# Optimization experiments

Hardware: AMD Instinct MI355X
Metric: run time of the kernel (lower is better)

Reference implementation:

```python
import jax, jax.numpy as jnp
import numpy as np
from jax import lax

B, C, H, W = 32, 128, 56, 56
O, KS, K = 128, 3, 2
HIDDEN = 32  # int(in_planes * ratio)
TEMPERATURE = 31.0
STRIDE, PAD = 1, 1


def setup_inputs() -> dict:
    key = jax.random.key(0)
    ks = jax.random.split(key, 6)
    return {
        "x": jax.random.normal(ks[0], (B, C, H, W), jnp.float32),
        "common_weight": jax.random.normal(ks[1], (1, O, C, KS, KS), jnp.float32) * 0.05,
        "common_bias": jax.random.normal(ks[2], (1, O), jnp.float32) * 0.05,
        "dyn_weight": jax.random.normal(ks[3], (1, O, C, KS, KS), jnp.float32) * 0.05,
        "dyn_bias": jnp.zeros((1, O), jnp.float32),
        "fc1_w": jax.random.normal(ks[4], (HIDDEN, C), jnp.float32) * 0.1,
        "fc2_w": jax.random.normal(ks[5], (K, HIDDEN), jnp.float32) * 0.1,
    }


def reference(x, common_weight, common_bias, dyn_weight, dyn_bias, fc1_w, fc2_w):
    b, c, h, w = x.shape
    # attention2d: global avg pool -> 1x1 conv -> relu -> 1x1 conv -> softmax(./T)
    pooled = jnp.mean(x, axis=(2, 3))                       # [B, C]
    hid = jax.nn.relu(pooled @ fc1_w.T)                     # [B, hidden]
    logits = hid @ fc2_w.T                                  # [B, K]
    attn = jax.nn.softmax(logits / TEMPERATURE, axis=1)     # [B, K]

    # aggregate per-sample weights/biases from the K-bank
    weight_all = jnp.concatenate([common_weight, dyn_weight], axis=0)  # [K,O,C,k,k]
    agg_w = jnp.einsum('bk,kocij->bocij', attn, weight_all)            # [B,O,C,k,k]
    bias_all = jnp.concatenate([common_bias, dyn_bias], axis=0)       # [K,O]
    agg_b = attn @ bias_all                                            # [B,O]

    # per-sample conv via grouped conv with feature_group_count = batch
    x1 = x.reshape(1, b * c, h, w)
    w1 = agg_w.reshape(b * O, c, KS, KS)
    out = lax.conv_general_dilated(
        x1, w1,
        window_strides=(STRIDE, STRIDE),
        padding=((PAD, PAD), (PAD, PAD)),
        dimension_numbers=('NCHW', 'OIHW', 'NCHW'),
        feature_group_count=b,
    )  # [1, B*O, H', W']
    out = out.reshape(b, O, out.shape[-2], out.shape[-1])
    return out + agg_b[:, :, None, None]
```

## Files before the change

### kernel.cpp

```cpp
#include <hip/hip_runtime.h>


#define B_ 32
#define C_ 128
#define O_ 128
#define SP_ 3136

typedef __bf16  bf16x8 __attribute__((ext_vector_type(8)));
typedef short   short8 __attribute__((ext_vector_type(8)));
typedef float   f32x4  __attribute__((ext_vector_type(4)));

__device__ __forceinline__ short f2bf(float f) {
  unsigned u = __float_as_uint(f);
  u += 0x7fffu + ((u >> 16) & 1u);
  return (short)(u >> 16);
}
__device__ __forceinline__ float bf2f(short s) {
  return __uint_as_float(((unsigned)(unsigned short)s) << 16);
}

#define GLOAD_LDS16(gp, lp)                                                     \
  __builtin_amdgcn_global_load_lds(                                             \
      (const __attribute__((address_space(1))) unsigned int*)(gp),              \
      (__attribute__((address_space(3))) unsigned int*)(lp), 16, 0, 0)

#define WS_PARTIAL_F 0
#define WS_ATTN_F    229376
#define WS_AGGB_F    229440
#define WS_ZERO_B    934144
#define WS_WB_B      935168
#define WS_XH_B      10372352
#define WS_NEED      36062464ull

__global__ __launch_bounds__(256) void convert_k(const float* __restrict__ x,
                                                 short* __restrict__ xh,
                                                 float* __restrict__ partial) {
  const int h = blockIdx.x, b = blockIdx.y;
  const int tid = threadIdx.x;
  __shared__ short lc[C_ * 57];
  const float* xp = x + (size_t)b * C_ * SP_ + h * 56;
#pragma unroll
  for (int q = 0; q < 7; ++q) {
    int i = q * 256 + tid;
    int c = i / 14, w4 = (i - c * 14) * 4;
    float4 v = *reinterpret_cast<const float4*>(xp + (size_t)c * SP_ + w4);
    lc[c * 57 + w4 + 0] = f2bf(v.x);
    lc[c * 57 + w4 + 1] = f2bf(v.y);
    lc[c * 57 + w4 + 2] = f2bf(v.z);
    lc[c * 57 + w4 + 3] = f2bf(v.w);
  }
  __syncthreads();
  if (tid < C_) {
    float s = 0.f;
    for (int w = 0; w < 56; ++w) s += bf2f(lc[tid * 57 + w]);
    partial[((size_t)b * 56 + h) * C_ + tid] = s;
  }
  short* xo = xh + ((size_t)b * 56 + h) * 56 * C_;
  for (int u = tid; u < 896; u += 256) {
    int w = u >> 4, cp = (u & 15) * 8;
    short8 v;
#pragma unroll
    for (int k = 0; k < 8; ++k) v[k] = lc[(cp + k) * 57 + w];
    *reinterpret_cast<short8*>(xo + w * C_ + cp) = v;
  }
}

__global__ __launch_bounds__(256) void pool_attn_k(const float* __restrict__ partial,
                                                   const float* __restrict__ fc1,
                                                   const float* __restrict__ fc2,
                                                   const float* __restrict__ cbias,
                                                   const float* __restrict__ dbias,
                                                   float* __restrict__ attn,
                                                   float* __restrict__ aggb) {
  const int b = blockIdx.x, tid = threadIdx.x;
  __shared__ float red[256];
  __shared__ float pooled_s[C_];
  __shared__ float hid[32];
  __shared__ float at[2];
  {
    const int c = tid & 127, half = tid >> 7;
    float s = 0.f;
    for (int hh = half * 28; hh < half * 28 + 28; ++hh)
      s += partial[((size_t)b * 56 + hh) * C_ + c];
    red[tid] = s;
  }
  __syncthreads();
  if (tid < C_) pooled_s[tid] = (red[tid] + red[tid + 128]) * (1.f / 3136.f);
  __syncthreads();
  if (tid < 32) {
    float s = 0.f;
    for (int c = 0; c < C_; ++c) s += pooled_s[c] * fc1[tid * C_ + c];
    hid[tid] = fmaxf(s, 0.f);
  }
  __syncthreads();
  if (tid == 0) {
    float l0 = 0.f, l1 = 0.f;
    for (int hh = 0; hh < 32; ++hh) {
      l0 += hid[hh] * fc2[hh];
      l1 += hid[hh] * fc2[32 + hh];
    }
    l0 *= (1.f / 31.f); l1 *= (1.f / 31.f);
    float m = fmaxf(l0, l1);
    float e0 = __expf(l0 - m), e1 = __expf(l1 - m);
    float inv = 1.f / (e0 + e1);
    at[0] = e0 * inv; at[1] = e1 * inv;
    attn[b * 2] = at[0]; attn[b * 2 + 1] = at[1];
  }
  __syncthreads();
  if (tid < C_)
    aggb[b * O_ + tid] = at[0] * cbias[tid] + at[1] * dbias[tid];
}

__global__ __launch_bounds__(256) void wagg_k(const float* __restrict__ w0,
                                              const float* __restrict__ w1,
                                              const float* __restrict__ attn,
                                              short* __restrict__ Wb) {
  const int b = blockIdx.x >> 3, og = blockIdx.x & 7;
  const int o0 = og * 16;
  const int tid = threadIdx.x;
  const float a0 = attn[b * 2], a1 = attn[b * 2 + 1];
  __shared__ short wl[9 * 16 * C_];
#pragma unroll
  for (int it = 0; it < 8; ++it) {
    int r = it * 256 + tid;
    int o = o0 + (r >> 7), c = r & 127;
    size_t base = ((size_t)o * C_ + c) * 9;
#pragma unroll
    for (int j = 0; j < 9; ++j) {
      float v = a0 * w0[base + j] + a1 * w1[base + j];
      wl[j * 2048 + r] = f2bf(v);
    }
  }
  __syncthreads();
#pragma unroll
  for (int it = 0; it < 9; ++it) {
    int u = it * 256 + tid;
    int ij = u >> 8, v = (u & 255) * 8;
    *reinterpret_cast<short8*>(Wb + (((size_t)b * 9 + ij) * O_ + o0) * C_ + v) =
        *reinterpret_cast<const short8*>(&wl[ij * 2048 + v]);
  }
}

#define TPOS 348
#define UNITS 1392
#define BUFB 22272
__global__ __launch_bounds__(256) void conv2_k(const char* __restrict__ wsbase,
                                               const short* __restrict__ Wb,
                                               const float* __restrict__ aggb,
                                               float* __restrict__ out) {
  const int flat = blockIdx.x;
  const int swz = (flat & 7) * 56 + (flat >> 3);
  const int b = swz / 14, ht = swz - b * 14;
  const int h0 = ht * 4;
  const int tid = threadIdx.x;
  const int lane = tid & 63, wv = tid >> 6;
  const int obase = (wv >> 1) * 64;
  const int nbase = (wv & 1) * 112;
  const int l15 = lane & 15, g = lane >> 4;

  __shared__ short xs[2 * BUFB / 2];

  int goff[6];
  bool gact[6];
#pragma unroll
  for (int it = 0; it < 6; ++it) {
    int u = tid + it * 256;
    gact[it] = (u < UNITS);
    int uu = gact[it] ? u : 0;
    int pos = uu >> 2;
    int spart = ((uu & 3) - (uu >> 4)) & 3;
    int r = pos / 58, wc = pos - r * 58;
    int h = h0 - 1 + r, w = wc - 1;
    bool val = (unsigned)h < 56u && (unsigned)w < 56u;
    goff[it] = val ? (int)(WS_XH_B + 2 * (((((b * 56 + h) * 56 + w)) << 7) + spart * 8))
                   : (int)WS_ZERO_B;
  }

  int ptile[7];
#pragma unroll
  for (int n = 0; n < 7; ++n) {
    int p = nbase + n * 16 + l15;
    int hl = p / 56, wl = p - hl * 56;
    ptile[n] = (hl + 1) * 58 + (wl + 1);
  }

  f32x4 acc[4][7];
#pragma unroll
  for (int m = 0; m < 4; ++m)
#pragma unroll
    for (int n = 0; n < 7; ++n) acc[m][n] = f32x4{0.f, 0.f, 0.f, 0.f};

#pragma unroll
  for (int it = 0; it < 6; ++it)
    if (gact[it])
      GLOAD_LDS16(wsbase + goff[it], (char*)xs + it * 4096 + wv * 1024);
  __syncthreads();

#pragma unroll
  for (int cc = 0; cc < 4; ++cc) {
    const int cur = cc & 1;
    if (cc < 3) {
      const int nb = cur ^ 1;
#pragma unroll
      for (int it = 0; it < 6; ++it)
        if (gact[it])
          GLOAD_LDS16(wsbase + goff[it] + (cc + 1) * 64,
                      (char*)xs + nb * BUFB + it * 4096 + wv * 1024);
    }
    const char* bp = (const char*)xs + cur * BUFB;
    const short* wbb = Wb + (((size_t)b * 9) << 14) + cc * 32 + g * 8;
#pragma unroll
    for (int ij = 0; ij < 9; ++ij) {
      const int sh = (ij / 3 - 1) * 58 + (ij % 3 - 1);
      bf16x8 af[4];
#pragma unroll
      for (int m = 0; m < 4; ++m)
        af[m] = *reinterpret_cast<const bf16x8*>(wbb + (ij << 14) + (obase + m * 16 + l15) * C_);
#pragma unroll
      for (int n = 0; n < 7; ++n) {
        int pp = ptile[n] + sh;
        int off = (pp << 6) + ((((pp >> 2) + g) & 3) << 4);
        bf16x8 bfr = *reinterpret_cast<const bf16x8*>(bp + off);
#pragma unroll
        for (int m = 0; m < 4; ++m)
          acc[m][n] = __builtin_amdgcn_mfma_f32_16x16x32_bf16(af[m], bfr, acc[m][n], 0, 0, 0);
      }
    }
    __syncthreads();
  }

  const int r4 = g * 4;
#pragma unroll
  for (int m = 0; m < 4; ++m) {
    float bias[4];
#pragma unroll
    for (int j = 0; j < 4; ++j) bias[j] = aggb[b * O_ + obase + m * 16 + r4 + j];
#pragma unroll
    for (int n = 0; n < 7; ++n) {
      int p = nbase + n * 16 + l15;
      int h = h0 + p / 56, w = p % 56;
#pragma unroll
      for (int j = 0; j < 4; ++j) {
        int o = obase + m * 16 + r4 + j;
        out[((size_t)(b * O_ + o) * 56 + h) * 56 + w] = acc[m][n][j] + bias[j];
      }
    }
  }
}

extern "C" void kernel_launch(void* const* d_in, const int* in_sizes, int n_in,
                              void* d_out, int out_size, void* d_ws, size_t ws_size,
                              hipStream_t stream) {
  const float* x    = (const float*)d_in[0];
  const float* cw   = (const float*)d_in[1];
  const float* cb   = (const float*)d_in[2];
  const float* dw   = (const float*)d_in[3];
  const float* db   = (const float*)d_in[4];
  const float* fc1  = (const float*)d_in[5];
  const float* fc2  = (const float*)d_in[6];
  float* out = (float*)d_out;

  char* wsb     = (char*)d_ws;
  float* partial = (float*)wsb + WS_PARTIAL_F;
  float* attn    = (float*)wsb + WS_ATTN_F;
  float* aggb    = (float*)wsb + WS_AGGB_F;
  short* Wb      = (short*)(wsb + WS_WB_B);
  short* xh      = (short*)(wsb + WS_XH_B);

  hipMemsetAsync(wsb + WS_ZERO_B, 0, 1024, stream);
  convert_k<<<dim3(56, B_), 256, 0, stream>>>(x, xh, partial);
  pool_attn_k<<<B_, 256, 0, stream>>>(partial, fc1, fc2, cb, db, attn, aggb);
  wagg_k<<<256, 256, 0, stream>>>(cw, dw, attn, Wb);
  conv2_k<<<448, 256, 0, stream>>>(wsb, Wb, aggb, out);
}
```

Baseline: 179.4 us.

## Stage conv weight tiles through double-buffered LDS and parallelize attention MLP

New measurement: 175.4 us. 1.02x faster.

```diff
diff --git a/kernel.cpp b/kernel.cpp
--- a/kernel.cpp
+++ b/kernel.cpp
@@ -30,7 +30,6 @@
 #define WS_ZERO_B    934144
 #define WS_WB_B      935168
 #define WS_XH_B      10372352
-#define WS_NEED      36062464ull
 
 __global__ __launch_bounds__(256) void convert_k(const float* __restrict__ x,
                                                  short* __restrict__ xh,
@@ -76,6 +75,7 @@
   __shared__ float red[256];
   __shared__ float pooled_s[C_];
   __shared__ float hid[32];
+  __shared__ float lg[2];
   __shared__ float at[2];
   {
     const int c = tid & 127, half = tid >> 7;
@@ -87,21 +87,38 @@
   __syncthreads();
   if (tid < C_) pooled_s[tid] = (red[tid] + red[tid + 128]) * (1.f / 3136.f);
   __syncthreads();
+  {
+    const int hd = tid >> 3, part = tid & 7;
+    const float4* fa = reinterpret_cast<const float4*>(fc1 + hd * C_ + part * 16);
+    const float4* pa = reinterpret_cast<const float4*>(pooled_s + part * 16);
+    float s = 0.f;
+#pragma unroll
+    for (int i = 0; i < 4; ++i) {
+      float4 f = fa[i], p = pa[i];
+      s += f.x * p.x + f.y * p.y + f.z * p.z + f.w * p.w;
+    }
+    red[tid] = s;
+  }
+  __syncthreads();
   if (tid < 32) {
-    float s = 0.f;
-    for (int c = 0; c < C_; ++c) s += pooled_s[c] * fc1[tid * C_ + c];
-    hid[tid] = fmaxf(s, 0.f);
+    float v = 0.f;
+#pragma unroll
+    for (int j = 0; j < 8; ++j) v += red[tid * 8 + j];
+    hid[tid] = fmaxf(v, 0.f);
+  }
+  __syncthreads();
+  if (tid < 64) red[tid] = hid[tid & 31] * fc2[tid];
+  __syncthreads();
+  if (tid < 2) {
+    float l = 0.f;
+#pragma unroll
+    for (int hh = 0; hh < 32; ++hh) l += red[tid * 32 + hh];
+    lg[tid] = l * (1.f / 31.f);
   }
   __syncthreads();
   if (tid == 0) {
-    float l0 = 0.f, l1 = 0.f;
-    for (int hh = 0; hh < 32; ++hh) {
-      l0 += hid[hh] * fc2[hh];
-      l1 += hid[hh] * fc2[32 + hh];
-    }
-    l0 *= (1.f / 31.f); l1 *= (1.f / 31.f);
-    float m = fmaxf(l0, l1);
-    float e0 = __expf(l0 - m), e1 = __expf(l1 - m);
+    float m = fmaxf(lg[0], lg[1]);
+    float e0 = __expf(lg[0] - m), e1 = __expf(lg[1] - m);
     float inv = 1.f / (e0 + e1);
     at[0] = e0 * inv; at[1] = e1 * inv;
     attn[b * 2] = at[0]; attn[b * 2 + 1] = at[1];
@@ -142,12 +159,13 @@
 }
 
 #define TPOS 348
-#define UNITS 1392
-#define BUFB 22272
-__global__ __launch_bounds__(256) void conv2_k(const char* __restrict__ wsbase,
-                                               const short* __restrict__ Wb,
-                                               const float* __restrict__ aggb,
-                                               float* __restrict__ out) {
+#define BUNITS 1392
+#define BBUF 22272
+#define AOFF 44544
+#define ABUF 8192
+__global__ __launch_bounds__(256, 2) void conv3_k(const char* __restrict__ wsbase,
+                                                  const float* __restrict__ aggb,
+                                                  float* __restrict__ out) {
   const int flat = blockIdx.x;
   const int swz = (flat & 7) * 56 + (flat >> 3);
   const int b = swz / 14, ht = swz - b * 14;
@@ -158,24 +176,37 @@
   const int nbase = (wv & 1) * 112;
   const int l15 = lane & 15, g = lane >> 4;
 
-  __shared__ short xs[2 * BUFB / 2];
-
-  int goff[6];
+  __shared__ __align__(16) char xs[AOFF + 2 * ABUF];
+
+  const char* gsrcB[6];
   bool gact[6];
 #pragma unroll
   for (int it = 0; it < 6; ++it) {
     int u = tid + it * 256;
-    gact[it] = (u < UNITS);
+    gact[it] = (u < BUNITS);
     int uu = gact[it] ? u : 0;
     int pos = uu >> 2;
-    int spart = ((uu & 3) - (uu >> 4)) & 3;
+    int q = ((uu & 3) - (uu >> 4)) & 3;
     int r = pos / 58, wc = pos - r * 58;
     int h = h0 - 1 + r, w = wc - 1;
     bool val = (unsigned)h < 56u && (unsigned)w < 56u;
-    goff[it] = val ? (int)(WS_XH_B + 2 * (((((b * 56 + h) * 56 + w)) << 7) + spart * 8))
-                   : (int)WS_ZERO_B;
-  }
-
+    gsrcB[it] = wsbase + (val ? (WS_XH_B + 2 * ((((b * 56 + h) * 56 + w) << 7) + q * 8))
+                              : WS_ZERO_B);
+  }
+  const char* gsrcA[2];
+#pragma unroll
+  for (int it = 0; it < 2; ++it) {
+    int u = tid + it * 256;
+    int o = u >> 2;
+    int q = ((u & 3) - (u >> 4)) & 3;
+    gsrcA[it] = wsbase + WS_WB_B + 2 * ((size_t)b * 147456 + o * C_ + q * 8);
+  }
+  int aoffR[4];
+#pragma unroll
+  for (int m = 0; m < 4; ++m) {
+    int o = obase + m * 16 + l15;
+    aoffR[m] = (o << 6) + (((g + (o >> 2)) & 3) << 4);
+  }
   int ptile[7];
 #pragma unroll
   for (int n = 0; n < 7; ++n) {
@@ -192,41 +223,55 @@
 
 #pragma unroll
   for (int it = 0; it < 6; ++it)
-    if (gact[it])
-      GLOAD_LDS16(wsbase + goff[it], (char*)xs + it * 4096 + wv * 1024);
-  __syncthreads();
+    if (gact[it]) GLOAD_LDS16(gsrcB[it], xs + it * 4096 + wv * 1024);
+#pragma unroll
+  for (int it = 0; it < 2; ++it)
+    GLOAD_LDS16(gsrcA[it], xs + AOFF + it * 4096 + wv * 1024);
+  asm volatile("s_waitcnt vmcnt(0)" ::: "memory");
+  __builtin_amdgcn_s_barrier();
 
 #pragma unroll
   for (int cc = 0; cc < 4; ++cc) {
-    const int cur = cc & 1;
-    if (cc < 3) {
-      const int nb = cur ^ 1;
-#pragma unroll
-      for (int it = 0; it < 6; ++it)
-        if (gact[it])
-          GLOAD_LDS16(wsbase + goff[it] + (cc + 1) * 64,
-                      (char*)xs + nb * BUFB + it * 4096 + wv * 1024);
-    }
-    const char* bp = (const char*)xs + cur * BUFB;
-    const short* wbb = Wb + (((size_t)b * 9) << 14) + cc * 32 + g * 8;
 #pragma unroll
     for (int ij = 0; ij < 9; ++ij) {
+      const int s = cc * 9 + ij;
+      const int apar = s & 1, bpar = cc & 1;
+      if (s < 35) {
+        const int s2 = s + 1, cc2 = s2 / 9, ij2 = s2 - cc2 * 9;
+        const int adelta = 2 * (ij2 * 16384 + cc2 * 32);
+#pragma unroll
+        for (int it = 0; it < 2; ++it)
+          GLOAD_LDS16(gsrcA[it] + adelta,
+                      xs + AOFF + ((s2 & 1) ? ABUF : 0) + it * 4096 + wv * 1024);
+      }
+      if (ij == 0 && cc < 3) {
+#pragma unroll
+        for (int it = 0; it < 6; ++it)
+          if (gact[it])
+            GLOAD_LDS16(gsrcB[it] + (cc + 1) * 64,
+                        xs + (bpar ? 0 : BBUF) + it * 4096 + wv * 1024);
+      }
+      const char* abuf = xs + AOFF + (apar ? ABUF : 0);
+      const char* bbuf = xs + (bpar ? BBUF : 0);
+      bf16x8 af[4];
+#pragma unroll
+      for (int m = 0; m < 4; ++m)
+        af[m] = *reinterpret_cast<const bf16x8*>(abuf + aoffR[m]);
       const int sh = (ij / 3 - 1) * 58 + (ij % 3 - 1);
-      bf16x8 af[4];
-#pragma unroll
-      for (int m = 0; m < 4; ++m)
-        af[m] = *reinterpret_cast<const bf16x8*>(wbb + (ij << 14) + (obase + m * 16 + l15) * C_);
 #pragma unroll
       for (int n = 0; n < 7; ++n) {
         int pp = ptile[n] + sh;
         int off = (pp << 6) + ((((pp >> 2) + g) & 3) << 4);
-        bf16x8 bfr = *reinterpret_cast<const bf16x8*>(bp + off);
+        bf16x8 bfr = *reinterpret_cast<const bf16x8*>(bbuf + off);
 #pragma unroll
         for (int m = 0; m < 4; ++m)
           acc[m][n] = __builtin_amdgcn_mfma_f32_16x16x32_bf16(af[m], bfr, acc[m][n], 0, 0, 0);
       }
+      if (s < 35) {
+        asm volatile("s_waitcnt vmcnt(0)" ::: "memory");
+        __builtin_amdgcn_s_barrier();
+      }
     }
-    __syncthreads();
   }
 
   const int r4 = g * 4;
@@ -260,7 +305,7 @@
   const float* fc2  = (const float*)d_in[6];
   float* out = (float*)d_out;
 
-  char* wsb     = (char*)d_ws;
+  char* wsb      = (char*)d_ws;
   float* partial = (float*)wsb + WS_PARTIAL_F;
   float* attn    = (float*)wsb + WS_ATTN_F;
   float* aggb    = (float*)wsb + WS_AGGB_F;
@@ -271,5 +316,5 @@
   convert_k<<<dim3(56, B_), 256, 0, stream>>>(x, xh, partial);
   pool_attn_k<<<B_, 256, 0, stream>>>(partial, fc1, fc2, cb, db, attn, aggb);
   wagg_k<<<256, 256, 0, stream>>>(cw, dw, attn, Wb);
-  conv2_k<<<448, 256, 0, stream>>>(wsb, Wb, aggb, out);
-}
+  conv3_k<<<448, 256, 0, stream>>>(wsb, aggb, out);
+}
```
